# Optimization experiments

Measured on AMD Instinct MI355X. Metric: run time of the kernel, lower is better.

The kernel has to match this reference:

```python
import jax, jax.numpy as jnp
import numpy as np

P, E, D = 128, 32, 64          # n_proxy_sets, n_elements, d
B, SEG_LEN = 1024, 128          # number of segments, per-segment length
N = B * SEG_LEN                 # total elements


def setup_inputs() -> dict:
    key = jax.random.key(0)
    k_x, k_p = jax.random.split(key)
    x = jax.random.normal(k_x, (N, D), dtype=jnp.float32)
    proxy_sets = jax.random.normal(k_p, (P, E, D), dtype=jnp.float32)
    index = jnp.full((B,), SEG_LEN, dtype=jnp.int32)  # segment lengths, sum == N
    return {"x": x, "proxy_sets": proxy_sets, "index": index}


def reference(x, proxy_sets, index):
    # sim_mat[p,e,n] = proxy_sets[p,e,:] . x[n,:]
    sim = jnp.einsum("ped,nd->pen", proxy_sets, x)     # [P,E,N]
    t = jnp.max(sim, axis=1)                             # [P,N]  max over proxy elements
    # ragged segment sum over N driven by segment lengths `index`
    seg_ids = jnp.repeat(jnp.arange(B, dtype=jnp.int32), index,
                         total_repeat_length=N)          # [N]
    pooled = jax.ops.segment_sum(t.T, seg_ids, num_segments=B)  # [B,P]
    pooled = pooled.astype(jnp.float32)
    # F.normalize(p=2, dim=1): divide by max(||.||_2, eps)
    norm = jnp.linalg.norm(pooled, axis=1, keepdims=True)
    return pooled / jnp.maximum(norm, 1e-12)
```

## Files before the change

### kernel.cpp

```cpp
#include <hip/hip_runtime.h>
#include <stdint.h>


typedef short short8 __attribute__((ext_vector_type(8)));
typedef __bf16 bf16x8 __attribute__((ext_vector_type(8)));
typedef float floatx16 __attribute__((ext_vector_type(16)));

#define NELEM 32
#define DIM   64
#define NSEG  1024
#define BROW  36

__device__ __forceinline__ unsigned short f32_to_bf16_rne(float f) {
  union { float f; unsigned int u; } v; v.f = f;
  unsigned int r = v.u + 0x7fffu + ((v.u >> 16) & 1u);
  return (unsigned short)(r >> 16);
}

__global__ void sc_prep(const float* __restrict__ proxy,
                        const int* __restrict__ index,
                        short* __restrict__ pb2,
                        int* __restrict__ offs) {
  const int bx = blockIdx.x, t = threadIdx.x;
  if (bx == 0) {
    __shared__ int lsum[256];
    const int base = t * 4;
    const int i0 = index[base + 0], i1 = index[base + 1];
    const int i2 = index[base + 2], i3 = index[base + 3];
    const int s = i0 + i1 + i2 + i3;
    lsum[t] = s;
    __syncthreads();
    for (int off = 1; off < 256; off <<= 1) {
      int v = (t >= off) ? lsum[t - off] : 0;
      __syncthreads();
      lsum[t] += v;
      __syncthreads();
    }
    const int ex = lsum[t] - s;
    offs[base + 0] = ex;
    offs[base + 1] = ex + i0;
    offs[base + 2] = ex + i0 + i1;
    offs[base + 3] = ex + i0 + i1 + i2;
    if (t == 255) offs[NSEG] = ex + s;
  } else {
    const int w = t >> 6, lane = t & 63;
    const int task = (bx - 1) * 4 + w;
    const int p = task >> 2, kk = task & 3;
    const int l31 = lane & 31, h = lane >> 5;
    const float* src = proxy + (size_t)p * (NELEM * DIM) + l31 * DIM + kk * 16 + h * 8;
    float4 f0 = *(const float4*)(src);
    float4 f1 = *(const float4*)(src + 4);
    short8 fr;
    fr[0] = (short)f32_to_bf16_rne(f0.x);
    fr[1] = (short)f32_to_bf16_rne(f0.y);
    fr[2] = (short)f32_to_bf16_rne(f0.z);
    fr[3] = (short)f32_to_bf16_rne(f0.w);
    fr[4] = (short)f32_to_bf16_rne(f1.x);
    fr[5] = (short)f32_to_bf16_rne(f1.y);
    fr[6] = (short)f32_to_bf16_rne(f1.z);
    fr[7] = (short)f32_to_bf16_rne(f1.w);
    *(short8*)(pb2 + ((size_t)task * 64 + lane) * 8) = fr;
  }
}

__device__ __forceinline__ float max16(const floatx16& a) {
  float r0 = fmaxf(fmaxf(a[0], a[1]), a[2]);
  float r1 = fmaxf(fmaxf(a[3], a[4]), a[5]);
  float r2 = fmaxf(fmaxf(a[6], a[7]), a[8]);
  float r3 = fmaxf(fmaxf(a[9], a[10]), a[11]);
  float r4 = fmaxf(fmaxf(a[12], a[13]), a[14]);
  float r5 = fmaxf(fmaxf(r0, r1), r2);
  float r6 = fmaxf(fmaxf(r3, r4), a[15]);
  return fmaxf(r5, r6);
}

__global__ __launch_bounds__(256, 2) void sc_main(
    const float* __restrict__ x,
    const short* __restrict__ pb2,
    const int* __restrict__ offs,
    float* __restrict__ out,
    int nrows) {
  __shared__ float buf[128 * BROW];
  __shared__ float red[4];

  const int b = blockIdx.x;
  const int tid = threadIdx.x;
  const int lane = tid & 63;
  const int w = tid >> 6;
  const int l31 = lane & 31;
  const int h = lane >> 5;

  const int start = offs[b];
  const int end = offs[b + 1];
  const int len = end - start;
  const int first = start >> 5;
  const int ntiles = (len > 0) ? (((end + 31) >> 5) - first) : 0;
  const int npass = (ntiles + 3) >> 2;

  if (ntiles == 0) {
    for (int j = tid; j < 128 * BROW; j += 256) buf[j] = 0.f;
  }

  floatx16 zc;
#pragma unroll
  for (int r = 0; r < 16; ++r) zc[r] = 0.f;

  const short* abase = pb2 + ((size_t)w * 4 * 64 + lane) * 8;

  for (int pass = 0; pass < npass; ++pass) {
    short8 bfrag[4][4];
    bool vmask[4];
#pragma unroll
    for (int t4 = 0; t4 < 4; ++t4) {
      const int tile = first + pass * 4 + t4;
      const int n = tile * 32 + l31;
      vmask[t4] = (n >= start) && (n < end);
      int rn = n < nrows ? n : nrows - 1;
      const float* xr = x + (size_t)rn * DIM + h * 8;
#pragma unroll
      for (int kk = 0; kk < 4; ++kk) {
        float4 f0 = *(const float4*)(xr + kk * 16);
        float4 f1 = *(const float4*)(xr + kk * 16 + 4);
        short8 fr;
        fr[0] = (short)f32_to_bf16_rne(f0.x);
        fr[1] = (short)f32_to_bf16_rne(f0.y);
        fr[2] = (short)f32_to_bf16_rne(f0.z);
        fr[3] = (short)f32_to_bf16_rne(f0.w);
        fr[4] = (short)f32_to_bf16_rne(f1.x);
        fr[5] = (short)f32_to_bf16_rne(f1.y);
        fr[6] = (short)f32_to_bf16_rne(f1.z);
        fr[7] = (short)f32_to_bf16_rne(f1.w);
        bfrag[t4][kk] = fr;
      }
    }

    auto process = [&](int i, short8 (&cur)[4], short8 (&nxt)[4], bool pf) {
      if (pf) {
        const short* ap = abase + (size_t)(i + 1) * 8192;
#pragma unroll
        for (int kk = 0; kk < 4; ++kk)
          nxt[kk] = *(const short8*)(ap + kk * 512);
      }
      floatx16 a0, a1, a2, a3;
#pragma unroll
      for (int kk = 0; kk < 4; ++kk) {
        bf16x8 a = __builtin_bit_cast(bf16x8, cur[kk]);
        bf16x8 b0 = __builtin_bit_cast(bf16x8, bfrag[0][kk]);
        bf16x8 b1 = __builtin_bit_cast(bf16x8, bfrag[1][kk]);
        bf16x8 b2 = __builtin_bit_cast(bf16x8, bfrag[2][kk]);
        bf16x8 b3 = __builtin_bit_cast(bf16x8, bfrag[3][kk]);
        if (kk == 0) {
          a0 = __builtin_amdgcn_mfma_f32_32x32x16_bf16(a, b0, zc, 0, 0, 0);
          a1 = __builtin_amdgcn_mfma_f32_32x32x16_bf16(a, b1, zc, 0, 0, 0);
          a2 = __builtin_amdgcn_mfma_f32_32x32x16_bf16(a, b2, zc, 0, 0, 0);
          a3 = __builtin_amdgcn_mfma_f32_32x32x16_bf16(a, b3, zc, 0, 0, 0);
        } else {
          a0 = __builtin_amdgcn_mfma_f32_32x32x16_bf16(a, b0, a0, 0, 0, 0);
          a1 = __builtin_amdgcn_mfma_f32_32x32x16_bf16(a, b1, a1, 0, 0, 0);
          a2 = __builtin_amdgcn_mfma_f32_32x32x16_bf16(a, b2, a2, 0, 0, 0);
          a3 = __builtin_amdgcn_mfma_f32_32x32x16_bf16(a, b3, a3, 0, 0, 0);
        }
      }
      float m0 = max16(a0), m1 = max16(a1), m2 = max16(a2), m3 = max16(a3);
      m0 = fmaxf(m0, __shfl_xor(m0, 32, 64));
      m1 = fmaxf(m1, __shfl_xor(m1, 32, 64));
      m2 = fmaxf(m2, __shfl_xor(m2, 32, 64));
      m3 = fmaxf(m3, __shfl_xor(m3, 32, 64));
      m0 = vmask[0] ? m0 : 0.f;
      m1 = vmask[1] ? m1 : 0.f;
      m2 = vmask[2] ? m2 : 0.f;
      m3 = vmask[3] ? m3 : 0.f;
      const float s = (m0 + m1) + (m2 + m3);
      if (h == 0) {
        const int p = w + 4 * i;
        const int idx = p * BROW + l31;
        float prev = (pass == 0) ? 0.f : buf[idx];
        buf[idx] = prev + s;
      }
    };

    short8 afA[4], afB[4];
#pragma unroll
    for (int kk = 0; kk < 4; ++kk)
      afA[kk] = *(const short8*)(abase + kk * 512);
    for (int i = 0; i < 32; i += 2) {
      process(i, afA, afB, true);
      process(i + 1, afB, afA, i < 30);
    }
  }
  __syncthreads();

  const int p2 = tid >> 1, part = tid & 1;
  const float* bp = buf + p2 * BROW + part * 16;
  float4 v0 = *(const float4*)(bp + 0);
  float4 v1 = *(const float4*)(bp + 4);
  float4 v2 = *(const float4*)(bp + 8);
  float4 v3 = *(const float4*)(bp + 12);
  float s16 = ((v0.x + v0.y) + (v0.z + v0.w)) + ((v1.x + v1.y) + (v1.z + v1.w)) +
              ((v2.x + v2.y) + (v2.z + v2.w)) + ((v3.x + v3.y) + (v3.z + v3.w));
  const float s32 = s16 + __shfl_xor(s16, 1, 64);

  float sq = part ? 0.f : s32 * s32;
#pragma unroll
  for (int off = 1; off <= 32; off <<= 1) sq += __shfl_xor(sq, off, 64);
  if (lane == 0) red[w] = sq;
  __syncthreads();
  const float ss = (red[0] + red[1]) + (red[2] + red[3]);
  const float inv = 1.f / fmaxf(sqrtf(ss), 1e-12f);
  if (part == 0) out[(b << 7) + p2] = s32 * inv;
}

extern "C" void kernel_launch(void* const* d_in, const int* in_sizes, int n_in,
                              void* d_out, int out_size, void* d_ws, size_t ws_size,
                              hipStream_t stream) {
  (void)n_in; (void)out_size; (void)ws_size;
  const float* x = (const float*)d_in[0];
  const float* proxy = (const float*)d_in[1];
  const int* index = (const int*)d_in[2];
  float* out = (float*)d_out;
  const int nrows = in_sizes[0] / DIM;

  int* offs = (int*)d_ws;
  short* pb2 = (short*)((char*)d_ws + 8192);

  sc_prep<<<129, 256, 0, stream>>>(proxy, index, pb2, offs);
  sc_main<<<NSEG, 256, 0, stream>>>(x, pb2, offs, out, nrows);
}
```

Measured before the change: 137.7 us.

## Software-pipeline MFMA groups so max-reduction epilogue overlaps next MFMA chain

```diff
diff --git a/kernel.cpp b/kernel.cpp
--- a/kernel.cpp
+++ b/kernel.cpp
@@ -10,6 +10,10 @@
 #define DIM   64
 #define NSEG  1024
 #define BROW  36
+
+#define MFMA_B16(d, a, b, c) \
+  d = __builtin_amdgcn_mfma_f32_32x32x16_bf16((a), (b), (c), 0, 0, 0)
+#define BC(v) __builtin_bit_cast(bf16x8, v)
 
 __device__ __forceinline__ unsigned short f32_to_bf16_rne(float f) {
   union { float f; unsigned int u; } v; v.f = f;
@@ -134,58 +138,122 @@
       }
     }
 
-    auto process = [&](int i, short8 (&cur)[4], short8 (&nxt)[4], bool pf) {
+    short8 afA[4], afB[4];
+    floatx16 xa, xb, ya, yb;
+    float n0 = 0.f, n1 = 0.f;
+
+    auto g0 = [&](int i, short8 (&cur)[4], short8 (&nxt)[4], bool pf, bool epi,
+                  float pn0, float pn1) {
       if (pf) {
         const short* ap = abase + (size_t)(i + 1) * 8192;
 #pragma unroll
         for (int kk = 0; kk < 4; ++kk)
           nxt[kk] = *(const short8*)(ap + kk * 512);
       }
-      floatx16 a0, a1, a2, a3;
-#pragma unroll
-      for (int kk = 0; kk < 4; ++kk) {
-        bf16x8 a = __builtin_bit_cast(bf16x8, cur[kk]);
-        bf16x8 b0 = __builtin_bit_cast(bf16x8, bfrag[0][kk]);
-        bf16x8 b1 = __builtin_bit_cast(bf16x8, bfrag[1][kk]);
-        bf16x8 b2 = __builtin_bit_cast(bf16x8, bfrag[2][kk]);
-        bf16x8 b3 = __builtin_bit_cast(bf16x8, bfrag[3][kk]);
-        if (kk == 0) {
-          a0 = __builtin_amdgcn_mfma_f32_32x32x16_bf16(a, b0, zc, 0, 0, 0);
-          a1 = __builtin_amdgcn_mfma_f32_32x32x16_bf16(a, b1, zc, 0, 0, 0);
-          a2 = __builtin_amdgcn_mfma_f32_32x32x16_bf16(a, b2, zc, 0, 0, 0);
-          a3 = __builtin_amdgcn_mfma_f32_32x32x16_bf16(a, b3, zc, 0, 0, 0);
-        } else {
-          a0 = __builtin_amdgcn_mfma_f32_32x32x16_bf16(a, b0, a0, 0, 0, 0);
-          a1 = __builtin_amdgcn_mfma_f32_32x32x16_bf16(a, b1, a1, 0, 0, 0);
-          a2 = __builtin_amdgcn_mfma_f32_32x32x16_bf16(a, b2, a2, 0, 0, 0);
-          a3 = __builtin_amdgcn_mfma_f32_32x32x16_bf16(a, b3, a3, 0, 0, 0);
+      float m2, m3;
+      {
+        const bf16x8 a = BC(cur[0]);
+        MFMA_B16(xa, a, BC(bfrag[0][0]), zc);
+        MFMA_B16(xb, a, BC(bfrag[1][0]), zc);
+      }
+      if (epi) m2 = max16(ya);
+      {
+        const bf16x8 a = BC(cur[1]);
+        MFMA_B16(xa, a, BC(bfrag[0][1]), xa);
+        MFMA_B16(xb, a, BC(bfrag[1][1]), xb);
+      }
+      if (epi) m3 = max16(yb);
+      {
+        const bf16x8 a = BC(cur[2]);
+        MFMA_B16(xa, a, BC(bfrag[0][2]), xa);
+        MFMA_B16(xb, a, BC(bfrag[1][2]), xb);
+      }
+      if (epi) {
+        m2 = fmaxf(m2, __shfl_xor(m2, 32, 64));
+        m3 = fmaxf(m3, __shfl_xor(m3, 32, 64));
+      }
+      {
+        const bf16x8 a = BC(cur[3]);
+        MFMA_B16(xa, a, BC(bfrag[0][3]), xa);
+        MFMA_B16(xb, a, BC(bfrag[1][3]), xb);
+      }
+      if (epi) {
+        m2 = vmask[2] ? m2 : 0.f;
+        m3 = vmask[3] ? m3 : 0.f;
+        const float s = (pn0 + pn1) + (m2 + m3);
+        if (h == 0) {
+          const int idx = (w + 4 * (i - 1)) * BROW + l31;
+          float prev = (pass == 0) ? 0.f : buf[idx];
+          buf[idx] = prev + s;
         }
       }
-      float m0 = max16(a0), m1 = max16(a1), m2 = max16(a2), m3 = max16(a3);
+    };
+
+    auto g1 = [&](short8 (&cur)[4]) {
+      float m0, m1;
+      {
+        const bf16x8 a = BC(cur[0]);
+        MFMA_B16(ya, a, BC(bfrag[2][0]), zc);
+        MFMA_B16(yb, a, BC(bfrag[3][0]), zc);
+      }
+      m0 = max16(xa);
+      {
+        const bf16x8 a = BC(cur[1]);
+        MFMA_B16(ya, a, BC(bfrag[2][1]), ya);
+        MFMA_B16(yb, a, BC(bfrag[3][1]), yb);
+      }
+      m1 = max16(xb);
+      {
+        const bf16x8 a = BC(cur[2]);
+        MFMA_B16(ya, a, BC(bfrag[2][2]), ya);
+        MFMA_B16(yb, a, BC(bfrag[3][2]), yb);
+      }
       m0 = fmaxf(m0, __shfl_xor(m0, 32, 64));
       m1 = fmaxf(m1, __shfl_xor(m1, 32, 64));
+      {
+        const bf16x8 a = BC(cur[3]);
+        MFMA_B16(ya, a, BC(bfrag[2][3]), ya);
+        MFMA_B16(yb, a, BC(bfrag[3][3]), yb);
+      }
+      n0 = vmask[0] ? m0 : 0.f;
+      n1 = vmask[1] ? m1 : 0.f;
+    };
+
+#pragma unroll
+    for (int kk = 0; kk < 4; ++kk)
+      afA[kk] = *(const short8*)(abase + kk * 512);
+    {
+      const short* ap = abase + 8192;
+#pragma unroll
+      for (int kk = 0; kk < 4; ++kk)
+        afB[kk] = *(const short8*)(ap + kk * 512);
+    }
+    g0(0, afA, afB, false, false, 0.f, 0.f);
+    g1(afA);
+
+#pragma unroll 1
+    for (int k = 0; k < 15; ++k) {
+      const int i = 2 * k + 1;
+      g0(i, afB, afA, true, true, n0, n1);
+      g1(afB);
+      g0(i + 1, afA, afB, true, true, n0, n1);
+      g1(afA);
+    }
+    g0(31, afB, afA, false, true, n0, n1);
+    g1(afB);
+
+    {
+      float m2 = max16(ya), m3 = max16(yb);
       m2 = fmaxf(m2, __shfl_xor(m2, 32, 64));
       m3 = fmaxf(m3, __shfl_xor(m3, 32, 64));
-      m0 = vmask[0] ? m0 : 0.f;
-      m1 = vmask[1] ? m1 : 0.f;
       m2 = vmask[2] ? m2 : 0.f;
       m3 = vmask[3] ? m3 : 0.f;
-      const float s = (m0 + m1) + (m2 + m3);
+      const float s = (n0 + n1) + (m2 + m3);
       if (h == 0) {
-        const int p = w + 4 * i;
-        const int idx = p * BROW + l31;
+        const int idx = (w + 4 * 31) * BROW + l31;
         float prev = (pass == 0) ? 0.f : buf[idx];
         buf[idx] = prev + s;
       }
-    };
-
-    short8 afA[4], afB[4];
-#pragma unroll
-    for (int kk = 0; kk < 4; ++kk)
-      afA[kk] = *(const short8*)(abase + kk * 512);
-    for (int i = 0; i < 32; i += 2) {
-      process(i, afA, afB, true);
-      process(i + 1, afB, afA, i < 30);
     }
   }
   __syncthreads();
```

Measured after the change: 130.9 us. 5.0% less time.
